# Kernel tuning notes

Measured on AMD Instinct MI355X. Metric: run time of the kernel, lower is better.

## Reference

```python
import jax, jax.numpy as jnp
import numpy as np

B, S, E, H = 4, 2048, 2048, 16
D = E // H  # head_dim = 128


def setup_inputs() -> dict:
    key = jax.random.key(0)
    kx, kq, kk, kv = jax.random.split(key, 4)
    std = 1.0 / np.sqrt(E)
    return {
        "x": jax.random.normal(kx, (B, S, E), dtype=jnp.float32),
        "Wq": jax.random.normal(kq, (E, E), dtype=jnp.float32) * std,
        "Wk": jax.random.normal(kk, (E, E), dtype=jnp.float32) * std,
        "Wv": jax.random.normal(kv, (E, E), dtype=jnp.float32) * std,
    }


def reference(x, Wq, Wk, Wv):
    b, s, _ = x.shape
    # nn.Linear(bias=False): y = x @ W.T
    q = (x @ Wq.T).reshape(b, s, H, D).transpose(0, 2, 1, 3)  # [b,h,s,d]
    k = (x @ Wk.T).reshape(b, s, H, D).transpose(0, 2, 1, 3)
    v = (x @ Wv.T).reshape(b, s, H, D).transpose(0, 2, 1, 3)
    scale = jnp.sqrt(jnp.asarray(D, dtype=jnp.float32))
    scores = jnp.einsum("bhqd,bhkd->bhqk", q, k) / scale  # [b,h,s,s]
    causal = jnp.tril(jnp.ones((s, s), dtype=bool))
    scores = jnp.where(causal, scores, -jnp.inf)
    weights = jax.nn.softmax(scores, axis=-1)
    attn = jnp.einsum("bhqk,bhkd->bhqd", weights, v)  # [b,h,s,d]
    return attn
```

## Files before the change

### kernel.cpp

```cpp
#include <hip/hip_runtime.h>
#include <hip/hip_bf16.h>
#include <stdint.h>

#define Bdim 4
#define Sdim 2048
#define Edim 2048
#define Hdim 16
#define Ddim 128

typedef unsigned short u16;
typedef unsigned int u32;
typedef __attribute__((ext_vector_type(8))) short bf16x8;
typedef __attribute__((ext_vector_type(4))) float f32x4;
typedef __attribute__((ext_vector_type(16))) float f32x16;
typedef __attribute__((ext_vector_type(4))) unsigned short u16x4;

__device__ inline u16 f2bf(float f) {
  union { float f; uint32_t u; } v; v.f = f;
  uint32_t u = v.u;
  return (u16)((u + 0x7FFFu + ((u >> 16) & 1u)) >> 16);
}

__device__ inline u32 pkbf(float lo, float hi) {
  float2 t; t.x = lo; t.y = hi;
  union { __hip_bfloat162 h2; u32 u; } cv;
  cv.h2 = __float22bfloat162_rn(t);
  return cv.u;
}

__device__ inline f32x4 mfma16(bf16x8 a, bf16x8 b, f32x4 c) {
  return __builtin_amdgcn_mfma_f32_16x16x32_bf16(a, b, c, 0, 0, 0);
}
__device__ inline f32x16 mfma32(bf16x8 a, bf16x8 b, f32x16 c) {
  return __builtin_amdgcn_mfma_f32_32x32x16_bf16(a, b, c, 0, 0, 0);
}

__device__ inline void load_lds16(const void* g, const void* l) {
  __builtin_amdgcn_global_load_lds(
      (__attribute__((address_space(1))) void*)(uintptr_t)g,
      (__attribute__((address_space(3))) void*)(uint32_t)(uintptr_t)l,
      16, 0, 0);
}

__global__ void cvt_kernel(const float* __restrict__ src, u16* __restrict__ dst, int n4) {
  int i = blockIdx.x * blockDim.x + threadIdx.x;
  if (i < n4) {
    float4 f = ((const float4*)src)[i];
    u16x4 o = { f2bf(f.x), f2bf(f.y), f2bf(f.z), f2bf(f.w) };
    ((u16x4*)dst)[i] = o;
  }
}

template <bool TRANSV>
__global__ __launch_bounds__(512, 2)
void gemm_nt(const u16* __restrict__ A, const u16* __restrict__ Bw,
             u16* __restrict__ C, int M, int N, int K) {
  __shared__ char lds[131072];

  const int tid = threadIdx.x;
  const int lane = tid & 63;
  const int w = tid >> 6;
  const int wm = w >> 2, wn = w & 3;
  const int bm = blockIdx.x, bn = blockIdx.y;
  const int NT = K >> 5;

  const int srow_off = lane >> 2;
  const int schunk = lane & 3;

  const int l15 = lane & 15;
  const int l4 = lane >> 4;
  const int rA = wm * 128 + l15;
  const int rB = wn * 64 + l15;
  const int gA = (rA + (rA >> 2)) & 3;
  const int gB = (rB + (rB >> 2)) & 3;
  const int aoff = rA * 64 + ((l4 ^ gA) << 4);
  const int boff = rB * 64 + ((l4 ^ gB) << 4);

  const u16* Agp = A + (size_t)(bm * 256) * K;
  const u16* Bgp = Bw + (size_t)(bn * 256) * K;

  f32x4 acc[8][4];
#pragma unroll
  for (int m = 0; m < 8; ++m)
#pragma unroll
    for (int n = 0; n < 4; ++n)
      acc[m][n] = (f32x4){0.f, 0.f, 0.f, 0.f};

#define GSTAGE(tt)                                                             \
  {                                                                            \
    const int slot_ = (tt) & 3;                                                \
    char* ab_ = lds + slot_ * 16384;                                           \
    char* bb_ = lds + 65536 + slot_ * 16384;                                   \
    _Pragma("unroll")                                                          \
    for (int i_ = 0; i_ < 2; ++i_) {                                           \
      const int rbase_ = w * 32 + i_ * 16;                                     \
      const int row_ = rbase_ + srow_off;                                      \
      const int src_ = schunk ^ ((row_ + (row_ >> 2)) & 3);                    \
      load_lds16(Agp + (size_t)row_ * K + (tt) * 32 + src_ * 8,                \
                 ab_ + rbase_ * 64);                                           \
      load_lds16(Bgp + (size_t)row_ * K + (tt) * 32 + src_ * 8,                \
                 bb_ + rbase_ * 64);                                           \
    }                                                                          \
  }

  GSTAGE(0);
  GSTAGE(1);
  asm volatile("s_waitcnt vmcnt(4)" ::: "memory");
  __builtin_amdgcn_s_barrier();

  for (int t = 0; t < NT; ++t) {
    if (t + 2 < NT) GSTAGE(t + 2);

    const char* ab = lds + (t & 3) * 16384 + aoff;
    const char* bb = lds + 65536 + (t & 3) * 16384 + boff;
    bf16x8 bfr[4];
#pragma unroll
    for (int n = 0; n < 4; ++n) bfr[n] = *(const bf16x8*)(bb + n * 1024);
    __builtin_amdgcn_s_setprio(1);
#pragma unroll
    for (int m = 0; m < 8; ++m) {
      bf16x8 af = *(const bf16x8*)(ab + m * 1024);
#pragma unroll
      for (int n = 0; n < 4; ++n) acc[m][n] = mfma16(af, bfr[n], acc[m][n]);
    }
    __builtin_amdgcn_s_setprio(0);

    if (t + 2 < NT) {
      asm volatile("s_waitcnt vmcnt(4)" ::: "memory");
      __builtin_amdgcn_s_barrier();
    } else if (t + 2 == NT) {
      asm volatile("s_waitcnt vmcnt(0)" ::: "memory");
      __builtin_amdgcn_s_barrier();
    }
  }
#undef GSTAGE

  const int r0 = bm * 256 + wm * 128 + (l4 << 2);
  const int c0 = bn * 256 + wn * 64 + l15;
  if (!TRANSV) {
#pragma unroll
    for (int m = 0; m < 8; ++m)
#pragma unroll
      for (int n = 0; n < 4; ++n) {
        int r = r0 + m * 16;
        int c = c0 + n * 16;
#pragma unroll
        for (int j = 0; j < 4; ++j)
          C[(size_t)(r + j) * N + c] = f2bf(acc[m][n][j]);
      }
  } else {
#pragma unroll
    for (int m = 0; m < 8; ++m)
#pragma unroll
      for (int n = 0; n < 4; ++n) {
        int ng = c0 + n * 16;
        int h = ng >> 7, d = ng & 127;
        int mg = r0 + m * 16;
        int b = mg >> 11, s = mg & 2047;
        u16x4 pk = { f2bf(acc[m][n][0]), f2bf(acc[m][n][1]),
                     f2bf(acc[m][n][2]), f2bf(acc[m][n][3]) };
        *(u16x4*)(C + ((size_t)((b * Hdim + h) * Ddim + d)) * Sdim + s) = pk;
      }
  }
}

__global__ __launch_bounds__(256)
void attn_kernel(const u16* __restrict__ Q, const u16* __restrict__ K,
                 const u16* __restrict__ Vt, float* __restrict__ O) {
  __shared__ u16 Ks[2][64 * 128];
  __shared__ u16 Vs[2][128 * 64];

  const int tid = threadIdx.x;
  const int lane = tid & 63;
  const int w = tid >> 6;
  const int l31 = lane & 31;
  const int hi = lane >> 5;

  const int bid = blockIdx.x;
  const int bh = bid & 63;
  const int qg = 15 - (bid >> 6);
  const int q0 = qg * 128;
  const int qw0 = q0 + w * 32;
  const int b = bh >> 4, h = bh & 15;

  const u16* Qb = Q + (size_t)b * Sdim * Edim + h * Ddim;
  const u16* Kb = K + (size_t)b * Sdim * Edim + h * Ddim;
  const u16* Vb = Vt + (size_t)bh * Ddim * Sdim;

  bf16x8 qf[8];
  {
    const u16* qrow = Qb + (size_t)(qw0 + l31) * Edim + hi * 8;
#pragma unroll
    for (int c = 0; c < 8; ++c) qf[c] = *(const bf16x8*)(qrow + c * 16);
  }

  f32x16 oacc[4];
#pragma unroll
  for (int d = 0; d < 4; ++d)
#pragma unroll
    for (int i = 0; i < 16; ++i) oacc[d][i] = 0.f;

  float m2 = -1e30f, lsum = 0.f;
  const float K1SC = 0.08838834764831845f * 1.4426950408889634f;
  const int qrel = qw0 + l31;

  const int nt = 2 * qg + 2;
  const int ntw = (qw0 + 31) / 64 + 1;

  const int krow_off = (lane >> 4);
  const int kchunk = lane & 15;
  const int vrow_off = (lane >> 3);
  const int vchunk = lane & 7;

#define STAGE(bufi, tt)                                                        \
  {                                                                            \
    const int kv0s = (tt) * 64;                                                \
    _Pragma("unroll")                                                          \
    for (int i = 0; i < 4; ++i) {                                              \
      const int rbase = w * 16 + i * 4;                                        \
      const int row = rbase + krow_off;                                        \
      const int cs = kchunk ^ (row & 15);                                      \
      load_lds16(Kb + (size_t)(kv0s + row) * Edim + cs * 8,                    \
                 &Ks[bufi][rbase * 128]);                                      \
    }                                                                          \
    _Pragma("unroll")                                                          \
    for (int i = 0; i < 4; ++i) {                                              \
      const int rbase = w * 32 + i * 8;                                        \
      const int row = rbase + vrow_off;                                        \
      const int cs = vchunk ^ (row & 7);                                       \
      load_lds16(Vb + (size_t)row * Sdim + kv0s + cs * 8,                      \
                 &Vs[bufi][rbase * 64]);                                       \
    }                                                                          \
  }

  STAGE(0, 0);
  __syncthreads();

  for (int t = 0; t < nt; ++t) {
    const int cur = t & 1;
    if (t + 1 < nt) STAGE(cur ^ 1, t + 1);

    if (t < ntw) {
      const int kv0 = t * 64;

      f32x16 sc0, sc1;
#pragma unroll
      for (int i = 0; i < 16; ++i) { sc0[i] = 0.f; sc1[i] = 0.f; }
#pragma unroll
      for (int c = 0; c < 8; ++c) {
        const int ch = c * 2 + hi;
        const int r0r = l31;
        const int r1r = 32 + l31;
        bf16x8 kf0 = *(const bf16x8*)&Ks[cur][r0r * 128 + (ch ^ (r0r & 15)) * 8];
        bf16x8 kf1 = *(const bf16x8*)&Ks[cur][r1r * 128 + (ch ^ (r1r & 15)) * 8];
        sc0 = mfma32(kf0, qf[c], sc0);
        sc1 = mfma32(kf1, qf[c], sc1);
      }

      float psc[32];
      float ma = -1e30f, mb = -1e30f, mc = -1e30f, md = -1e30f;
      if (kv0 + 64 > qw0) {
#pragma unroll
        for (int r = 0; r < 16; ++r) {
          const int cr = (r & 3) + 8 * (r >> 2) + 4 * hi;
          float v0 = (kv0 + cr <= qrel) ? sc0[r] * K1SC : -1e30f;
          float v1 = (kv0 + 32 + cr <= qrel) ? sc1[r] * K1SC : -1e30f;
          psc[r] = v0; psc[16 + r] = v1;
          if ((r & 3) == 0) { ma = fmaxf(ma, fmaxf(v0, v1)); }
          else if ((r & 3) == 1) { mb = fmaxf(mb, fmaxf(v0, v1)); }
          else if ((r & 3) == 2) { mc = fmaxf(mc, fmaxf(v0, v1)); }
          else { md = fmaxf(md, fmaxf(v0, v1)); }
        }
      } else {
#pragma unroll
        for (int r = 0; r < 16; ++r) {
          float v0 = sc0[r] * K1SC;
          float v1 = sc1[r] * K1SC;
          psc[r] = v0; psc[16 + r] = v1;
          if ((r & 3) == 0) { ma = fmaxf(ma, fmaxf(v0, v1)); }
          else if ((r & 3) == 1) { mb = fmaxf(mb, fmaxf(v0, v1)); }
          else if ((r & 3) == 2) { mc = fmaxf(mc, fmaxf(v0, v1)); }
          else { md = fmaxf(md, fmaxf(v0, v1)); }
        }
      }
      float mt = fmaxf(fmaxf(ma, mb), fmaxf(mc, md));
      float mo = fmaxf(mt, __shfl_xor(mt, 32));

      if (__any(mo - m2 > 8.0f)) {
        float mnew = fmaxf(m2, mo);
        float corr = __builtin_amdgcn_exp2f(m2 - mnew);
        m2 = mnew;
        lsum *= corr;
#pragma unroll
        for (int d = 0; d < 4; ++d)
#pragma unroll
          for (int i = 0; i < 16; ++i) oacc[d][i] *= corr;
      }

      float rs0 = 0.f, rs1 = 0.f, rs2 = 0.f, rs3 = 0.f;
#pragma unroll
      for (int r = 0; r < 32; r += 4) {
        psc[r]     = __builtin_amdgcn_exp2f(psc[r] - m2);     rs0 += psc[r];
        psc[r + 1] = __builtin_amdgcn_exp2f(psc[r + 1] - m2); rs1 += psc[r + 1];
        psc[r + 2] = __builtin_amdgcn_exp2f(psc[r + 2] - m2); rs2 += psc[r + 2];
        psc[r + 3] = __builtin_amdgcn_exp2f(psc[r + 3] - m2); rs3 += psc[r + 3];
      }
      float rs = (rs0 + rs1) + (rs2 + rs3);
      rs += __shfl_xor(rs, 32);
      lsum += rs;

      u32 pk[16], sx[16];
#pragma unroll
      for (int i = 0; i < 16; ++i) pk[i] = pkbf(psc[2 * i], psc[2 * i + 1]);
#pragma unroll
      for (int i = 0; i < 16; ++i) sx[i] = __shfl_xor(pk[i], 32);
      bf16x8 pa[4];
#pragma unroll
      for (int t2 = 0; t2 < 2; ++t2)
#pragma unroll
        for (int q2 = 0; q2 < 2; ++q2) {
          const int base = t2 * 8 + q2 * 4;
          union { u32 w[4]; bf16x8 v; } cv;
          cv.w[0] = hi ? sx[base + 2] : pk[base + 0];
          cv.w[1] = hi ? sx[base + 3] : pk[base + 1];
          cv.w[2] = hi ? pk[base + 2] : sx[base + 0];
          cv.w[3] = hi ? pk[base + 3] : sx[base + 1];
          pa[t2 * 2 + q2] = cv.v;
        }

#pragma unroll
      for (int dblk = 0; dblk < 4; ++dblk) {
        const int row = dblk * 32 + l31;
#pragma unroll
        for (int ks = 0; ks < 4; ++ks) {
          const int ch = ks * 2 + hi;
          bf16x8 vf = *(const bf16x8*)&Vs[cur][row * 64 + (ch ^ (row & 7)) * 8];
          oacc[dblk] = mfma32(vf, pa[ks], oacc[dblk]);
        }
      }
    }

    __syncthreads();
  }

  float inv = 1.0f / lsum;
  float* Ob = O + ((size_t)bh * Sdim + qw0 + l31) * Ddim + hi * 4;
#pragma unroll
  for (int dblk = 0; dblk < 4; ++dblk)
#pragma unroll
    for (int g = 0; g < 4; ++g) {
      f32x4 o4 = { oacc[dblk][4 * g] * inv, oacc[dblk][4 * g + 1] * inv,
                   oacc[dblk][4 * g + 2] * inv, oacc[dblk][4 * g + 3] * inv };
      *(f32x4*)(Ob + dblk * 32 + g * 8) = o4;
    }
}

extern "C" void kernel_launch(void* const* d_in, const int* in_sizes, int n_in,
                              void* d_out, int out_size, void* d_ws, size_t ws_size,
                              hipStream_t stream) {
  const float* x  = (const float*)d_in[0];
  const float* Wq = (const float*)d_in[1];
  const float* Wk = (const float*)d_in[2];
  const float* Wv = (const float*)d_in[3];
  float* out = (float*)d_out;
  char* ws = (char*)d_ws;

  u16* xb  = (u16*)(ws);
  u16* wqb = (u16*)(ws + 33554432ull);
  u16* wkb = (u16*)(ws + 41943040ull);
  u16* wvb = (u16*)(ws + 50331648ull);
  u16* Qb  = (u16*)(ws + 58720256ull);
  u16* Kb  = (u16*)(ws + 92274688ull);
  u16* Vt  = (u16*)(ws + 125829120ull);

  const int nX = Bdim * Sdim * Edim;
  const int nW = Edim * Edim;
  cvt_kernel<<<(nX / 4 + 255) / 256, 256, 0, stream>>>(x, xb, nX / 4);
  cvt_kernel<<<(nW / 4 + 255) / 256, 256, 0, stream>>>(Wq, wqb, nW / 4);
  cvt_kernel<<<(nW / 4 + 255) / 256, 256, 0, stream>>>(Wk, wkb, nW / 4);
  cvt_kernel<<<(nW / 4 + 255) / 256, 256, 0, stream>>>(Wv, wvb, nW / 4);

  dim3 g(Bdim * Sdim / 256, Edim / 256);
  gemm_nt<false><<<g, 512, 0, stream>>>(xb, wqb, Qb, Bdim * Sdim, Edim, Edim);
  gemm_nt<false><<<g, 512, 0, stream>>>(xb, wkb, Kb, Bdim * Sdim, Edim, Edim);
  gemm_nt<true ><<<g, 512, 0, stream>>>(xb, wvb, Vt, Bdim * Sdim, Edim, Edim);

  attn_kernel<<<Bdim * Hdim * (Sdim / 128), 256, 0, stream>>>(Qb, Kb, Vt, out);
}
```

Baseline: 392.2 us.

## Fold softmax scale into Wq, use permlane32 swaps and MFMA row sums

The softmax scale times log2(e) is folded into the Wq bf16 conversion, so the attention kernel no longer multiplies every score. Cross-half max and P-fragment exchanges now use permlane32_swap instead of __shfl_xor, which drops the 16 per-tile shuffles of packed P. Row sums come from an extra MFMA against a ones vector rather than VALU adds plus a shuffle. This cuts VALU and LDS-crossbar work in the softmax inner loop, at the cost of extra MFMA issue, an extra 16-float accumulator register block, and bf16 rounding in both the scaled Q and the row sums.

```diff
diff --git a/kernel.cpp b/kernel.cpp
--- a/kernel.cpp
+++ b/kernel.cpp
@@ -14,6 +14,7 @@
 typedef __attribute__((ext_vector_type(4))) float f32x4;
 typedef __attribute__((ext_vector_type(16))) float f32x16;
 typedef __attribute__((ext_vector_type(4))) unsigned short u16x4;
+typedef __attribute__((ext_vector_type(2))) unsigned int u32x2;
 
 __device__ inline u16 f2bf(float f) {
   union { float f; uint32_t u; } v; v.f = f;
@@ -42,11 +43,13 @@
       16, 0, 0);
 }
 
-__global__ void cvt_kernel(const float* __restrict__ src, u16* __restrict__ dst, int n4) {
+__global__ void cvt_kernel(const float* __restrict__ src, u16* __restrict__ dst,
+                           int n4, float scale) {
   int i = blockIdx.x * blockDim.x + threadIdx.x;
   if (i < n4) {
     float4 f = ((const float4*)src)[i];
-    u16x4 o = { f2bf(f.x), f2bf(f.y), f2bf(f.z), f2bf(f.w) };
+    u16x4 o = { f2bf(f.x * scale), f2bf(f.y * scale),
+                f2bf(f.z * scale), f2bf(f.w * scale) };
     ((u16x4*)dst)[i] = o;
   }
 }
@@ -199,9 +202,14 @@
   for (int d = 0; d < 4; ++d)
 #pragma unroll
     for (int i = 0; i < 16; ++i) oacc[d][i] = 0.f;
-
-  float m2 = -1e30f, lsum = 0.f;
-  const float K1SC = 0.08838834764831845f * 1.4426950408889634f;
+  f32x16 lacc;
+#pragma unroll
+  for (int i = 0; i < 16; ++i) lacc[i] = 0.f;
+
+  const short oneb = (short)0x3F80;
+  const bf16x8 ones = {oneb, oneb, oneb, oneb, oneb, oneb, oneb, oneb};
+
+  float m2 = -1e30f;
   const int qrel = qw0 + l31;
 
   const int nt = 2 * qg + 2;
@@ -263,68 +271,61 @@
 #pragma unroll
         for (int r = 0; r < 16; ++r) {
           const int cr = (r & 3) + 8 * (r >> 2) + 4 * hi;
-          float v0 = (kv0 + cr <= qrel) ? sc0[r] * K1SC : -1e30f;
-          float v1 = (kv0 + 32 + cr <= qrel) ? sc1[r] * K1SC : -1e30f;
+          float v0 = (kv0 + cr <= qrel) ? sc0[r] : -1e30f;
+          float v1 = (kv0 + 32 + cr <= qrel) ? sc1[r] : -1e30f;
           psc[r] = v0; psc[16 + r] = v1;
-          if ((r & 3) == 0) { ma = fmaxf(ma, fmaxf(v0, v1)); }
-          else if ((r & 3) == 1) { mb = fmaxf(mb, fmaxf(v0, v1)); }
-          else if ((r & 3) == 2) { mc = fmaxf(mc, fmaxf(v0, v1)); }
-          else { md = fmaxf(md, fmaxf(v0, v1)); }
+          if ((r & 3) == 0) { ma = fmaxf(fmaxf(ma, v0), v1); }
+          else if ((r & 3) == 1) { mb = fmaxf(fmaxf(mb, v0), v1); }
+          else if ((r & 3) == 2) { mc = fmaxf(fmaxf(mc, v0), v1); }
+          else { md = fmaxf(fmaxf(md, v0), v1); }
         }
       } else {
 #pragma unroll
         for (int r = 0; r < 16; ++r) {
-          float v0 = sc0[r] * K1SC;
-          float v1 = sc1[r] * K1SC;
+          float v0 = sc0[r];
+          float v1 = sc1[r];
           psc[r] = v0; psc[16 + r] = v1;
-          if ((r & 3) == 0) { ma = fmaxf(ma, fmaxf(v0, v1)); }
-          else if ((r & 3) == 1) { mb = fmaxf(mb, fmaxf(v0, v1)); }
-          else if ((r & 3) == 2) { mc = fmaxf(mc, fmaxf(v0, v1)); }
-          else { md = fmaxf(md, fmaxf(v0, v1)); }
+          if ((r & 3) == 0) { ma = fmaxf(fmaxf(ma, v0), v1); }
+          else if ((r & 3) == 1) { mb = fmaxf(fmaxf(mb, v0), v1); }
+          else if ((r & 3) == 2) { mc = fmaxf(fmaxf(mc, v0), v1); }
+          else { md = fmaxf(fmaxf(md, v0), v1); }
         }
       }
       float mt = fmaxf(fmaxf(ma, mb), fmaxf(mc, md));
-      float mo = fmaxf(mt, __shfl_xor(mt, 32));
+      u32x2 mx = __builtin_amdgcn_permlane32_swap(
+          __float_as_uint(mt), __float_as_uint(mt), false, false);
+      float mo = fmaxf(__uint_as_float(mx.x), __uint_as_float(mx.y));
 
       if (__any(mo - m2 > 8.0f)) {
         float mnew = fmaxf(m2, mo);
         float corr = __builtin_amdgcn_exp2f(m2 - mnew);
         m2 = mnew;
-        lsum *= corr;
+        lacc[0] *= corr;
 #pragma unroll
         for (int d = 0; d < 4; ++d)
 #pragma unroll
           for (int i = 0; i < 16; ++i) oacc[d][i] *= corr;
       }
 
-      float rs0 = 0.f, rs1 = 0.f, rs2 = 0.f, rs3 = 0.f;
-#pragma unroll
-      for (int r = 0; r < 32; r += 4) {
-        psc[r]     = __builtin_amdgcn_exp2f(psc[r] - m2);     rs0 += psc[r];
-        psc[r + 1] = __builtin_amdgcn_exp2f(psc[r + 1] - m2); rs1 += psc[r + 1];
-        psc[r + 2] = __builtin_amdgcn_exp2f(psc[r + 2] - m2); rs2 += psc[r + 2];
-        psc[r + 3] = __builtin_amdgcn_exp2f(psc[r + 3] - m2); rs3 += psc[r + 3];
-      }
-      float rs = (rs0 + rs1) + (rs2 + rs3);
-      rs += __shfl_xor(rs, 32);
-      lsum += rs;
-
-      u32 pk[16], sx[16];
+#pragma unroll
+      for (int r = 0; r < 32; ++r)
+        psc[r] = __builtin_amdgcn_exp2f(psc[r] - m2);
+
+      u32 pk[16];
 #pragma unroll
       for (int i = 0; i < 16; ++i) pk[i] = pkbf(psc[2 * i], psc[2 * i + 1]);
-#pragma unroll
-      for (int i = 0; i < 16; ++i) sx[i] = __shfl_xor(pk[i], 32);
       bf16x8 pa[4];
 #pragma unroll
       for (int t2 = 0; t2 < 2; ++t2)
 #pragma unroll
         for (int q2 = 0; q2 < 2; ++q2) {
           const int base = t2 * 8 + q2 * 4;
-          union { u32 w[4]; bf16x8 v; } cv;
-          cv.w[0] = hi ? sx[base + 2] : pk[base + 0];
-          cv.w[1] = hi ? sx[base + 3] : pk[base + 1];
-          cv.w[2] = hi ? pk[base + 2] : sx[base + 0];
-          cv.w[3] = hi ? pk[base + 3] : sx[base + 1];
+          u32x2 r0 = __builtin_amdgcn_permlane32_swap(pk[base + 0], pk[base + 2],
+                                                      false, false);
+          u32x2 r1 = __builtin_amdgcn_permlane32_swap(pk[base + 1], pk[base + 3],
+                                                      false, false);
+          union { u32 wv[4]; bf16x8 v; } cv;
+          cv.wv[0] = r0.x; cv.wv[1] = r1.x; cv.wv[2] = r0.y; cv.wv[3] = r1.y;
           pa[t2 * 2 + q2] = cv.v;
         }
 
@@ -338,12 +339,14 @@
           oacc[dblk] = mfma32(vf, pa[ks], oacc[dblk]);
         }
       }
+#pragma unroll
+      for (int ks = 0; ks < 4; ++ks) lacc = mfma32(ones, pa[ks], lacc);
     }
 
     __syncthreads();
   }
 
-  float inv = 1.0f / lsum;
+  float inv = 1.0f / lacc[0];
   float* Ob = O + ((size_t)bh * Sdim + qw0 + l31) * Ddim + hi * 4;
 #pragma unroll
   for (int dblk = 0; dblk < 4; ++dblk)
@@ -375,10 +378,11 @@
 
   const int nX = Bdim * Sdim * Edim;
   const int nW = Edim * Edim;
-  cvt_kernel<<<(nX / 4 + 255) / 256, 256, 0, stream>>>(x, xb, nX / 4);
-  cvt_kernel<<<(nW / 4 + 255) / 256, 256, 0, stream>>>(Wq, wqb, nW / 4);
-  cvt_kernel<<<(nW / 4 + 255) / 256, 256, 0, stream>>>(Wk, wkb, nW / 4);
-  cvt_kernel<<<(nW / 4 + 255) / 256, 256, 0, stream>>>(Wv, wvb, nW / 4);
+  const float K1SC = 0.08838834764831845f * 1.4426950408889634f;
+  cvt_kernel<<<(nX / 4 + 255) / 256, 256, 0, stream>>>(x, xb, nX / 4, 1.0f);
+  cvt_kernel<<<(nW / 4 + 255) / 256, 256, 0, stream>>>(Wq, wqb, nW / 4, K1SC);
+  cvt_kernel<<<(nW / 4 + 255) / 256, 256, 0, stream>>>(Wk, wkb, nW / 4, 1.0f);
+  cvt_kernel<<<(nW / 4 + 255) / 256, 256, 0, stream>>>(Wv, wvb, nW / 4, 1.0f);
 
   dim3 g(Bdim * Sdim / 256, Edim / 256);
   gemm_nt<false><<<g, 512, 0, stream>>>(xb, wqb, Qb, Bdim * Sdim, Edim, Edim);
```

Result: faster. 374.3 us (-4.6%).
